# Performance work log

Hardware: AMD Instinct MI355X
Metric: run time of the kernel (lower is better)

## Reference

```python
import jax, jax.numpy as jnp
import numpy as np

PHI = 3.1415926 * 0.3   # Cosine_fMRI default phi (data_dim=-1 -> A=1)
MIN_NORM = 1e-15
PROJ_EPS = 4e-3         # float32 eps used by hyperbolic project


def _project(x, c):
    # Clip to the Poincare ball of curvature c (norm over last dim).
    norm = jnp.maximum(jnp.linalg.norm(x, axis=-1, keepdims=True), MIN_NORM)
    maxnorm = (1.0 - PROJ_EPS) / jnp.sqrt(c)
    return jnp.where(norm > maxnorm, x / norm * maxnorm, x)


def _logmap0(x, c):
    sqrt_c = jnp.sqrt(c)
    norm = jnp.maximum(jnp.linalg.norm(x, axis=-1, keepdims=True), MIN_NORM)
    arg = jnp.clip(sqrt_c * norm, -1.0 + MIN_NORM, 1.0 - MIN_NORM)
    return jnp.arctanh(arg) / (sqrt_c * norm) * x


def _fkernel(x, c):
    return _logmap0(_project(x, c), c)


def _act(x, a):
    # F.relu(x) + a * cos(x + phi)  (Cosine_fMRI with A=1)
    return jax.nn.relu(x) + a * jnp.cos(x + PHI)


def _corr_abs(data):
    # data: [B, T, N]; per-sample |corrcoef| between ROIs -> [B, N, N]
    xm = data - jnp.mean(data, axis=1, keepdims=True)
    cov = jnp.einsum('btn,btm->bnm', xm, xm)
    d = jnp.sqrt(jnp.diagonal(cov, axis1=-2, axis2=-1))  # [B, N]
    corr = cov / (d[:, :, None] * d[:, None, :])
    return jnp.abs(jnp.nan_to_num(corr))


def _normalize_adj(adj):
    # D^-1/2 (A+I) D^-1/2 per block (block-diag structure -> batched dense)
    B, N, _ = adj.shape
    A = adj + jnp.eye(N, dtype=adj.dtype)
    dinv = jnp.power(jnp.sum(A, axis=-1), -0.5)  # [B, N]
    return dinv[:, :, None] * A * dinv[:, None, :]


def setup_inputs() -> dict:
    key = jax.random.key(0)
    ks = jax.random.split(key, 3)
    B, T, N, H = 256, 240, 264, 256
    data = jax.random.normal(ks[0], (B, T, N), dtype=jnp.float32)
    # kaiming_uniform-style init for GCN weights
    b1w = np.sqrt(6.0 / N)
    b2w = np.sqrt(6.0 / H)
    W1 = jax.random.uniform(ks[1], (N, H), jnp.float32, -b1w, b1w)
    W2 = jax.random.uniform(ks[2], (H, H), jnp.float32, -b2w, b2w)
    b1 = jnp.zeros((H,), jnp.float32)
    b2 = jnp.zeros((H,), jnp.float32)
    return {"data": data, "W1": W1, "b1": b1, "W2": W2, "b2": b2}


def reference(data, W1, b1, W2, b2):
    c = jnp.float32(1.0)
    a = jnp.float32(0.5)  # a_fMRI
    adj = _corr_abs(data)          # [B, N, N]; also the input features
    L = _normalize_adj(adj)        # [B, N, N]
    # GCN layer 1: L @ (fea @ W1) + b1  (batched == block-diag sparse.mm)
    x1 = jnp.einsum('bij,bjh->bih', L, adj @ W1) + b1
    g1 = _act(_fkernel(x1, c), a)
    x2 = jnp.einsum('bij,bjh->bih', L, g1 @ W2) + b2
    g2 = _act(_fkernel(x2, c), a)  # [B, N, H]
    return g2, adj
```

## Files before the change

### kernel.cpp

```cpp
#include <hip/hip_runtime.h>
#include <hip/hip_bf16.h>
#include <math.h>

#define B_ 256
#define T_ 240
#define N_ 264
#define H_ 256
#define BN_ (B_ * N_)
#define PHI_ 0.94247778f
#define MAXNORM_ 0.996f

typedef short short8 __attribute__((ext_vector_type(8)));
typedef float f32x4 __attribute__((ext_vector_type(4)));
typedef unsigned short ushort4v __attribute__((ext_vector_type(4)));

__device__ inline unsigned short f2bf(float f) {
  __hip_bfloat16 h = __float2bfloat16(f);
  return *reinterpret_cast<unsigned short*>(&h);
}
__device__ inline float bf2f(unsigned short u) {
  unsigned int x = ((unsigned int)u) << 16;
  return __uint_as_float(x);
}

__global__ __launch_bounds__(256) void stats_kernel(
    const float* __restrict__ data, float* __restrict__ mean, float* __restrict__ rd) {
  int b = blockIdx.x;
  const float* db = data + (size_t)b * T_ * N_;
  for (int n = threadIdx.x; n < N_; n += blockDim.x) {
    float s = 0.f, ss = 0.f;
    for (int t = 0; t < T_; ++t) {
      float v = db[(size_t)t * N_ + n];
      s += v; ss += v * v;
    }
    float m = s / (float)T_;
    float var = ss - s * m;
    float d = sqrtf(fmaxf(var, 0.f));
    mean[b * N_ + n] = m;
    rd[b * N_ + n] = (d > 0.f) ? (1.f / d) : 0.f;
  }
}

__global__ __launch_bounds__(256) void zT_kernel(
    const float* __restrict__ data, const float* __restrict__ mean,
    const float* __restrict__ rd, unsigned short* __restrict__ z) {
  int b = blockIdx.y;
  int n0 = blockIdx.x * 64;
  __shared__ unsigned short zl[64][242];
  int lane = threadIdx.x & 63, wv = threadIdx.x >> 6;
  int n = n0 + lane;
  float m = 0.f, r = 0.f;
  if (n < N_) { m = mean[b * N_ + n]; r = rd[b * N_ + n]; }
  for (int t = wv; t < T_; t += 4) {
    float v = (n < N_) ? data[((size_t)b * T_ + t) * N_ + n] : 0.f;
    zl[lane][t] = f2bf((v - m) * r);
  }
  __syncthreads();
  int tid = threadIdx.x;
  for (int rr = 0; rr < 64; ++rr) {
    int nn = n0 + rr;
    if (nn >= N_) break;
    unsigned short val = (tid < T_) ? zl[rr][tid] : (unsigned short)0;
    z[((size_t)b * N_ + nn) * 256 + tid] = val;
  }
}

__global__ __launch_bounds__(256) void wtrans_kernel(
    const float* __restrict__ W, unsigned short* __restrict__ WT,
    int Jv, int Jpad) {
  int jt = blockIdx.x * 64, ht = blockIdx.y * 64;
  __shared__ float tile[64][65];
  int tid = threadIdx.x;
  for (int idx = tid; idx < 4096; idx += 256) {
    int jr = idx >> 6, hr = idx & 63;
    int j = jt + jr;
    tile[jr][hr] = (j < Jv) ? W[(size_t)j * H_ + ht + hr] : 0.f;
  }
  __syncthreads();
  for (int idx = tid; idx < 4096; idx += 256) {
    int hr = idx >> 6, jr = idx & 63;
    int j = jt + jr;
    if (j < Jpad) WT[(size_t)(ht + hr) * Jpad + j] = f2bf(tile[jr][hr]);
  }
}

__global__ __launch_bounds__(256) void dinv_kernel(
    const float* __restrict__ adj, float* __restrict__ dinv) {
  int row  = blockIdx.x * 4 + (threadIdx.x >> 6);
  int lane = threadIdx.x & 63;
  const float* r = adj + (size_t)row * N_;
  float s = 0.f;
  for (int j = lane; j < N_; j += 64) s += r[j];
#pragma unroll
  for (int off = 32; off; off >>= 1) s += __shfl_down(s, off);
  if (lane == 0) dinv[row] = 1.f / sqrtf(s + 1.f);
}

template<int EPI>
__global__ __launch_bounds__(256) void mfma_gemm_kernel(
    const unsigned short* __restrict__ A, int lda, long sA,
    const unsigned short* __restrict__ Bm, int ldb, long sB,
    int ksteps,
    float* __restrict__ outF, unsigned short* __restrict__ outB,
    const float* __restrict__ dinv, const float* __restrict__ bias) {
  int b = blockIdx.z;
  int i0 = blockIdx.y * 64;
  int n0 = blockIdx.x * 256;
  int tid = threadIdx.x;
  int w = tid >> 6, lane = tid & 63, g = lane >> 4, l4 = lane & 15;

  __shared__ short8 AsV[4 * 64];
  __shared__ short8 BsV[4 * 256];

  const unsigned short* Ab = A + (size_t)b * sA;
  const unsigned short* Bb = Bm + (size_t)b * sB;

  f32x4 acc[4][4];
#pragma unroll
  for (int x = 0; x < 4; ++x)
#pragma unroll
    for (int y = 0; y < 4; ++y) acc[x][y] = (f32x4){0.f, 0.f, 0.f, 0.f};

  int arow = tid >> 2, akg = tid & 3;
  for (int ks = 0; ks < ksteps; ++ks) {
    int k0 = ks * 32;
    short8 av = *(const short8*)(Ab + (size_t)(i0 + arow) * lda + k0 + akg * 8);
    short8 bv[4];
#pragma unroll
    for (int it = 0; it < 4; ++it) {
      int nn = n0 + arow + it * 64;
      bv[it] = *(const short8*)(Bb + (size_t)nn * ldb + k0 + akg * 8);
    }
    __syncthreads();
    AsV[akg * 64 + arow] = av;
#pragma unroll
    for (int it = 0; it < 4; ++it) BsV[akg * 256 + arow + it * 64] = bv[it];
    __syncthreads();
    short8 af[4], bfr[4];
#pragma unroll
    for (int fr = 0; fr < 4; ++fr) af[fr] = AsV[g * 64 + fr * 16 + l4];
#pragma unroll
    for (int fc = 0; fc < 4; ++fc) bfr[fc] = BsV[g * 256 + w * 64 + fc * 16 + l4];
#pragma unroll
    for (int fr = 0; fr < 4; ++fr)
#pragma unroll
      for (int fc = 0; fc < 4; ++fc)
        acc[fr][fc] = __builtin_amdgcn_mfma_f32_16x16x32_bf16(af[fr], bfr[fc], acc[fr][fc], 0, 0, 0);
  }

  if constexpr (EPI == 0) {
#pragma unroll
    for (int fr = 0; fr < 4; ++fr) {
      int rb = i0 + fr * 16 + g * 4;
#pragma unroll
      for (int fc = 0; fc < 4; ++fc) {
        int j = n0 + w * 64 + fc * 16 + l4;
#pragma unroll
        for (int reg = 0; reg < 4; ++reg) {
          int i = rb + reg;
          float v = fabsf(acc[fr][fc][reg]);
          if (i < N_ && j < N_) outF[((size_t)b * N_ + i) * N_ + j] = v;
          if (i < N_ && j < 288) outB[((size_t)b * N_ + i) * 288 + j] = f2bf(j < N_ ? v : 0.f);
        }
      }
    }
  }

  if constexpr (EPI == 1) {
#pragma unroll
    for (int fr = 0; fr < 4; ++fr) {
      int rb = i0 + fr * 16 + g * 4;
      if (rb < 288) {
        float dv[4];
#pragma unroll
        for (int reg = 0; reg < 4; ++reg) {
          int j = rb + reg;
          dv[reg] = (j < N_) ? dinv[b * N_ + j] : 0.f;
        }
#pragma unroll
        for (int fc = 0; fc < 4; ++fc) {
          int col = w * 64 + fc * 16 + l4;
          ushort4v pk;
#pragma unroll
          for (int reg = 0; reg < 4; ++reg)
            pk[reg] = f2bf(dv[reg] * acc[fr][fc][reg]);
          *(ushort4v*)(outB + ((size_t)b * H_ + col) * 288 + rb) = pk;
        }
      }
    }
  }

  if constexpr (EPI >= 2) {
    __shared__ float rs[64][4];
    float ratio[4][4];
#pragma unroll
    for (int fr = 0; fr < 4; ++fr) {
      int rb = i0 + fr * 16 + g * 4;
      float din[4];
#pragma unroll
      for (int reg = 0; reg < 4; ++reg) din[reg] = dinv[b * N_ + rb + reg];
#pragma unroll
      for (int fc = 0; fc < 4; ++fc) {
        int col = w * 64 + fc * 16 + l4;
        ushort4v dy = *(const ushort4v*)(Bb + (size_t)col * ldb + rb);
        float bias_v = bias[col];
#pragma unroll
        for (int reg = 0; reg < 4; ++reg) {
          float x = din[reg] * (acc[fr][fc][reg] + bf2f(dy[reg])) + bias_v;
          acc[fr][fc][reg] = x;
        }
      }
    }
#pragma unroll
    for (int fr = 0; fr < 4; ++fr) {
#pragma unroll
      for (int reg = 0; reg < 4; ++reg) {
        float s = 0.f;
#pragma unroll
        for (int fc = 0; fc < 4; ++fc) { float x = acc[fr][fc][reg]; s += x * x; }
        s += __shfl_xor(s, 1); s += __shfl_xor(s, 2);
        s += __shfl_xor(s, 4); s += __shfl_xor(s, 8);
        if (l4 == 0) rs[fr * 16 + g * 4 + reg][w] = s;
      }
    }
    __syncthreads();
#pragma unroll
    for (int fr = 0; fr < 4; ++fr)
#pragma unroll
      for (int reg = 0; reg < 4; ++reg) {
        int r = fr * 16 + g * 4 + reg;
        float tot = rs[r][0] + rs[r][1] + rs[r][2] + rs[r][3];
        float norm = fmaxf(sqrtf(tot), 1e-15f);
        float scale = (norm > MAXNORM_) ? (MAXNORM_ / norm) : 1.0f;
        float pn = fmaxf(fminf(norm, MAXNORM_), 1e-15f);
        ratio[fr][reg] = atanhf(pn) / pn * scale;
      }
#pragma unroll
    for (int fr = 0; fr < 4; ++fr) {
      int rb = i0 + fr * 16 + g * 4;
#pragma unroll
      for (int fc = 0; fc < 4; ++fc) {
        int col = w * 64 + fc * 16 + l4;
#pragma unroll
        for (int reg = 0; reg < 4; ++reg) {
          int row = rb + reg;
          if (row < N_) {
            float y = ratio[fr][reg] * acc[fr][fc][reg];
            float o = fmaxf(y, 0.f) + 0.5f * __cosf(y + PHI_);
            if constexpr (EPI == 2) outB[((size_t)b * N_ + row) * H_ + col] = f2bf(o);
            else                    outF[((size_t)b * N_ + row) * H_ + col] = o;
          }
        }
      }
    }
  }
}

extern "C" void kernel_launch(void* const* d_in, const int* in_sizes, int n_in,
                              void* d_out, int out_size, void* d_ws, size_t ws_size,
                              hipStream_t stream) {
  const float* data = (const float*)d_in[0];
  const float* W1   = (const float*)d_in[1];
  const float* b1   = (const float*)d_in[2];
  const float* W2   = (const float*)d_in[3];
  const float* b2   = (const float*)d_in[4];

  float* g2   = (float*)d_out;
  float* adjF = g2 + (size_t)B_ * N_ * H_;

  float* ws_f = (float*)d_ws;
  float* mean = ws_f;
  float* rd   = ws_f + BN_;
  float* dinv = ws_f + 2 * BN_;
  unsigned short* region1 = (unsigned short*)(ws_f + 3 * BN_);
  unsigned short* z    = region1;
  unsigned short* YT   = region1;
  unsigned short* W1T  = region1 + (size_t)B_ * H_ * 288;
  unsigned short* W2T  = W1T + (size_t)H_ * 288;
  unsigned short* adjB = W2T + (size_t)H_ * H_;
  unsigned short* g1bf = (unsigned short*)d_out;

  stats_kernel<<<B_, 256, 0, stream>>>(data, mean, rd);
  zT_kernel<<<dim3(5, B_), 256, 0, stream>>>(data, mean, rd, z);
  wtrans_kernel<<<dim3(5, 4), 256, 0, stream>>>(W1, W1T, N_, 288);
  wtrans_kernel<<<dim3(4, 4), 256, 0, stream>>>(W2, W2T, H_, 256);
  mfma_gemm_kernel<0><<<dim3(2, 5, B_), 256, 0, stream>>>(
      z, 256, (long)N_ * 256, z, 256, (long)N_ * 256, 8, adjF, adjB, nullptr, nullptr);
  dinv_kernel<<<BN_ / 4, 256, 0, stream>>>(adjF, dinv);
  mfma_gemm_kernel<1><<<dim3(1, 5, B_), 256, 0, stream>>>(
      adjB, 288, (long)N_ * 288, W1T, 288, 0L, 9, nullptr, YT, dinv, nullptr);
  mfma_gemm_kernel<2><<<dim3(1, 5, B_), 256, 0, stream>>>(
      adjB, 288, (long)N_ * 288, YT, 288, (long)H_ * 288, 9, nullptr, g1bf, dinv, b1);
  mfma_gemm_kernel<1><<<dim3(1, 5, B_), 256, 0, stream>>>(
      g1bf, 256, (long)N_ * 256, W2T, 256, 0L, 8, nullptr, YT, dinv, nullptr);
  mfma_gemm_kernel<3><<<dim3(1, 5, B_), 256, 0, stream>>>(
      adjB, 288, (long)N_ * 288, YT, 288, (long)H_ * 288, 9, g2, nullptr, dinv, b2);
}
```

Measured before the change: 551.1 us.

## Fuse stats into transpose, fold degree sums into corr GEMM, swizzle LDS

Merges the per-ROI mean/std computation into the z-transpose kernel via an LDS-staged tile. It also removes the separate dinv pass by atomically accumulating row sums of |corr| in the first GEMM epilogue, and computes 1/sqrt(1+sum) on the fly in later epilogues. The GEMM gains an XOR-swizzled LDS layout to cut bank conflicts, an XCD-aware workgroup remapping, clamped out-of-range A rows, and skipping of MFMA work for waves whose B columns are fully out of range. This adds a memset and float atomics (nondeterministic summation order), and re-evaluates sqrt per epilogue.

```diff
diff --git a/kernel.cpp b/kernel.cpp
--- a/kernel.cpp
+++ b/kernel.cpp
@@ -23,45 +23,45 @@
   return __uint_as_float(x);
 }
 
-__global__ __launch_bounds__(256) void stats_kernel(
-    const float* __restrict__ data, float* __restrict__ mean, float* __restrict__ rd) {
-  int b = blockIdx.x;
-  const float* db = data + (size_t)b * T_ * N_;
-  for (int n = threadIdx.x; n < N_; n += blockDim.x) {
+__device__ inline int swz16(int row, int kg) {
+  return row * 4 + ((kg ^ (row >> 1)) & 3);
+}
+
+__global__ __launch_bounds__(256) void zTs_kernel(
+    const float* __restrict__ data, unsigned short* __restrict__ z) {
+  int b = blockIdx.y;
+  int n0 = blockIdx.x * 64;
+  __shared__ float ld[240 * 65];
+  __shared__ float ps[4][64], pq[4][64];
+  __shared__ float mS[64], rS[64];
+  int tid = threadIdx.x, lane = tid & 63, wv = tid >> 6;
+  int n = n0 + lane;
+  bool nv = n < N_;
+  for (int t = wv; t < T_; t += 4)
+    ld[t * 65 + lane] = nv ? data[((size_t)b * T_ + t) * N_ + n] : 0.f;
+  __syncthreads();
+  {
+    int col = tid & 63, q = tid >> 6;
     float s = 0.f, ss = 0.f;
-    for (int t = 0; t < T_; ++t) {
-      float v = db[(size_t)t * N_ + n];
-      s += v; ss += v * v;
-    }
+    for (int t = q * 60; t < q * 60 + 60; ++t) { float v = ld[t * 65 + col]; s += v; ss += v * v; }
+    ps[q][col] = s; pq[q][col] = ss;
+  }
+  __syncthreads();
+  if (tid < 64) {
+    float s  = ps[0][tid] + ps[1][tid] + ps[2][tid] + ps[3][tid];
+    float ss = pq[0][tid] + pq[1][tid] + pq[2][tid] + pq[3][tid];
     float m = s / (float)T_;
     float var = ss - s * m;
     float d = sqrtf(fmaxf(var, 0.f));
-    mean[b * N_ + n] = m;
-    rd[b * N_ + n] = (d > 0.f) ? (1.f / d) : 0.f;
-  }
-}
-
-__global__ __launch_bounds__(256) void zT_kernel(
-    const float* __restrict__ data, const float* __restrict__ mean,
-    const float* __restrict__ rd, unsigned short* __restrict__ z) {
-  int b = blockIdx.y;
-  int n0 = blockIdx.x * 64;
-  __shared__ unsigned short zl[64][242];
-  int lane = threadIdx.x & 63, wv = threadIdx.x >> 6;
-  int n = n0 + lane;
-  float m = 0.f, r = 0.f;
-  if (n < N_) { m = mean[b * N_ + n]; r = rd[b * N_ + n]; }
-  for (int t = wv; t < T_; t += 4) {
-    float v = (n < N_) ? data[((size_t)b * T_ + t) * N_ + n] : 0.f;
-    zl[lane][t] = f2bf((v - m) * r);
+    mS[tid] = m;
+    rS[tid] = (d > 0.f) ? (1.f / d) : 0.f;
   }
   __syncthreads();
-  int tid = threadIdx.x;
-  for (int rr = 0; rr < 64; ++rr) {
-    int nn = n0 + rr;
-    if (nn >= N_) break;
-    unsigned short val = (tid < T_) ? zl[rr][tid] : (unsigned short)0;
-    z[((size_t)b * N_ + nn) * 256 + tid] = val;
+  int nrows = min(64, N_ - n0);
+  for (int rr = 0; rr < nrows; ++rr) {
+    float m = mS[rr], r = rS[rr];
+    unsigned short val = (tid < T_) ? f2bf((ld[tid * 65 + rr] - m) * r) : (unsigned short)0;
+    z[((size_t)(b * N_ + n0 + rr)) * 256 + tid] = val;
   }
 }
 
@@ -84,33 +84,28 @@
   }
 }
 
-__global__ __launch_bounds__(256) void dinv_kernel(
-    const float* __restrict__ adj, float* __restrict__ dinv) {
-  int row  = blockIdx.x * 4 + (threadIdx.x >> 6);
-  int lane = threadIdx.x & 63;
-  const float* r = adj + (size_t)row * N_;
-  float s = 0.f;
-  for (int j = lane; j < N_; j += 64) s += r[j];
-#pragma unroll
-  for (int off = 32; off; off >>= 1) s += __shfl_down(s, off);
-  if (lane == 0) dinv[row] = 1.f / sqrtf(s + 1.f);
-}
-
 template<int EPI>
 __global__ __launch_bounds__(256) void mfma_gemm_kernel(
-    const unsigned short* __restrict__ A, int lda, long sA,
-    const unsigned short* __restrict__ Bm, int ldb, long sB,
+    const unsigned short* __restrict__ A, int lda, long sA, int rowsA,
+    const unsigned short* __restrict__ Bm, int ldb, long sB, int validB,
     int ksteps,
     float* __restrict__ outF, unsigned short* __restrict__ outB,
-    const float* __restrict__ dinv, const float* __restrict__ bias) {
-  int b = blockIdx.z;
-  int i0 = blockIdx.y * 64;
-  int n0 = blockIdx.x * 256;
+    float* __restrict__ dsum, const float* __restrict__ bias) {
+  int gx = gridDim.x, gy = gridDim.y;
+  int flat = (blockIdx.z * gy + blockIdx.y) * gx + blockIdx.x;
+  int nwg = gx * gy * gridDim.z;
+  int q8 = nwg >> 3;
+  int id = (flat & 7) * q8 + (flat >> 3);
+  int bx = id % gx; int tq = id / gx;
+  int b = tq / gy;
+  int i0 = (tq % gy) * 64;
+  int n0 = bx * 256;
+
   int tid = threadIdx.x;
   int w = tid >> 6, lane = tid & 63, g = lane >> 4, l4 = lane & 15;
 
-  __shared__ short8 AsV[4 * 64];
-  __shared__ short8 BsV[4 * 256];
+  __shared__ short8 AsV[256];
+  __shared__ short8 BsV[1024];
 
   const unsigned short* Ab = A + (size_t)b * sA;
   const unsigned short* Bb = Bm + (size_t)b * sB;
@@ -122,36 +117,45 @@
     for (int y = 0; y < 4; ++y) acc[x][y] = (f32x4){0.f, 0.f, 0.f, 0.f};
 
   int arow = tid >> 2, akg = tid & 3;
+  int rA = min(i0 + arow, rowsA - 1);
+  const unsigned short* Aptr = Ab + (size_t)rA * lda + akg * 8;
+  bool wactive = (n0 + w * 64) < validB;
+  const short8 zero8 = {};
+
   for (int ks = 0; ks < ksteps; ++ks) {
     int k0 = ks * 32;
-    short8 av = *(const short8*)(Ab + (size_t)(i0 + arow) * lda + k0 + akg * 8);
+    short8 av = *(const short8*)(Aptr + k0);
     short8 bv[4];
 #pragma unroll
     for (int it = 0; it < 4; ++it) {
       int nn = n0 + arow + it * 64;
-      bv[it] = *(const short8*)(Bb + (size_t)nn * ldb + k0 + akg * 8);
+      bv[it] = (nn < validB) ? *(const short8*)(Bb + (size_t)nn * ldb + k0 + akg * 8) : zero8;
     }
     __syncthreads();
-    AsV[akg * 64 + arow] = av;
-#pragma unroll
-    for (int it = 0; it < 4; ++it) BsV[akg * 256 + arow + it * 64] = bv[it];
+    AsV[swz16(arow, akg)] = av;
+#pragma unroll
+    for (int it = 0; it < 4; ++it) BsV[swz16(arow + it * 64, akg)] = bv[it];
     __syncthreads();
-    short8 af[4], bfr[4];
-#pragma unroll
-    for (int fr = 0; fr < 4; ++fr) af[fr] = AsV[g * 64 + fr * 16 + l4];
-#pragma unroll
-    for (int fc = 0; fc < 4; ++fc) bfr[fc] = BsV[g * 256 + w * 64 + fc * 16 + l4];
-#pragma unroll
-    for (int fr = 0; fr < 4; ++fr)
-#pragma unroll
-      for (int fc = 0; fc < 4; ++fc)
-        acc[fr][fc] = __builtin_amdgcn_mfma_f32_16x16x32_bf16(af[fr], bfr[fc], acc[fr][fc], 0, 0, 0);
+    if (wactive) {
+      short8 af[4], bfr[4];
+#pragma unroll
+      for (int fr = 0; fr < 4; ++fr) af[fr] = AsV[swz16(fr * 16 + l4, g)];
+#pragma unroll
+      for (int fc = 0; fc < 4; ++fc) bfr[fc] = BsV[swz16(w * 64 + fc * 16 + l4, g)];
+#pragma unroll
+      for (int fr = 0; fr < 4; ++fr)
+#pragma unroll
+        for (int fc = 0; fc < 4; ++fc)
+          acc[fr][fc] = __builtin_amdgcn_mfma_f32_16x16x32_bf16(af[fr], bfr[fc], acc[fr][fc], 0, 0, 0);
+    }
   }
 
   if constexpr (EPI == 0) {
+    __shared__ float rsum[64][4];
 #pragma unroll
     for (int fr = 0; fr < 4; ++fr) {
       int rb = i0 + fr * 16 + g * 4;
+      float sr[4] = {0.f, 0.f, 0.f, 0.f};
 #pragma unroll
       for (int fc = 0; fc < 4; ++fc) {
         int j = n0 + w * 64 + fc * 16 + l4;
@@ -161,8 +165,23 @@
           float v = fabsf(acc[fr][fc][reg]);
           if (i < N_ && j < N_) outF[((size_t)b * N_ + i) * N_ + j] = v;
           if (i < N_ && j < 288) outB[((size_t)b * N_ + i) * 288 + j] = f2bf(j < N_ ? v : 0.f);
-        }
-      }
+          if (j < N_) sr[reg] += v;
+        }
+      }
+#pragma unroll
+      for (int reg = 0; reg < 4; ++reg) {
+        float s = sr[reg];
+        s += __shfl_xor(s, 1); s += __shfl_xor(s, 2);
+        s += __shfl_xor(s, 4); s += __shfl_xor(s, 8);
+        if (l4 == 0) rsum[fr * 16 + g * 4 + reg][w] = s;
+      }
+    }
+    __syncthreads();
+    if (tid < 64) {
+      int i = i0 + tid;
+      if (i < N_)
+        atomicAdd(&dsum[(size_t)b * N_ + i],
+                  rsum[tid][0] + rsum[tid][1] + rsum[tid][2] + rsum[tid][3]);
     }
   }
 
@@ -175,7 +194,7 @@
 #pragma unroll
         for (int reg = 0; reg < 4; ++reg) {
           int j = rb + reg;
-          dv[reg] = (j < N_) ? dinv[b * N_ + j] : 0.f;
+          dv[reg] = (j < N_) ? (1.f / sqrtf(1.f + dsum[(size_t)b * N_ + j])) : 0.f;
         }
 #pragma unroll
         for (int fc = 0; fc < 4; ++fc) {
@@ -196,13 +215,17 @@
 #pragma unroll
     for (int fr = 0; fr < 4; ++fr) {
       int rb = i0 + fr * 16 + g * 4;
+      int rbc = min(rb, 284);
       float din[4];
 #pragma unroll
-      for (int reg = 0; reg < 4; ++reg) din[reg] = dinv[b * N_ + rb + reg];
+      for (int reg = 0; reg < 4; ++reg) {
+        int ic = min(rb + reg, N_ - 1);
+        din[reg] = 1.f / sqrtf(1.f + dsum[(size_t)b * N_ + ic]);
+      }
 #pragma unroll
       for (int fc = 0; fc < 4; ++fc) {
         int col = w * 64 + fc * 16 + l4;
-        ushort4v dy = *(const ushort4v*)(Bb + (size_t)col * ldb + rb);
+        ushort4v dy = *(const ushort4v*)(Bb + (size_t)col * ldb + rbc);
         float bias_v = bias[col];
 #pragma unroll
         for (int reg = 0; reg < 4; ++reg) {
@@ -269,10 +292,8 @@
   float* adjF = g2 + (size_t)B_ * N_ * H_;
 
   float* ws_f = (float*)d_ws;
-  float* mean = ws_f;
-  float* rd   = ws_f + BN_;
-  float* dinv = ws_f + 2 * BN_;
-  unsigned short* region1 = (unsigned short*)(ws_f + 3 * BN_);
+  float* dsum = ws_f;
+  unsigned short* region1 = (unsigned short*)(ws_f + BN_);
   unsigned short* z    = region1;
   unsigned short* YT   = region1;
   unsigned short* W1T  = region1 + (size_t)B_ * H_ * 288;
@@ -280,19 +301,23 @@
   unsigned short* adjB = W2T + (size_t)H_ * H_;
   unsigned short* g1bf = (unsigned short*)d_out;
 
-  stats_kernel<<<B_, 256, 0, stream>>>(data, mean, rd);
-  zT_kernel<<<dim3(5, B_), 256, 0, stream>>>(data, mean, rd, z);
+  hipMemsetAsync(dsum, 0, BN_ * sizeof(float), stream);
+  zTs_kernel<<<dim3(5, B_), 256, 0, stream>>>(data, z);
   wtrans_kernel<<<dim3(5, 4), 256, 0, stream>>>(W1, W1T, N_, 288);
   wtrans_kernel<<<dim3(4, 4), 256, 0, stream>>>(W2, W2T, H_, 256);
   mfma_gemm_kernel<0><<<dim3(2, 5, B_), 256, 0, stream>>>(
-      z, 256, (long)N_ * 256, z, 256, (long)N_ * 256, 8, adjF, adjB, nullptr, nullptr);
-  dinv_kernel<<<BN_ / 4, 256, 0, stream>>>(adjF, dinv);
+      z, 256, (long)N_ * 256, N_, z, 256, (long)N_ * 256, N_, 8,
+      adjF, adjB, dsum, nullptr);
   mfma_gemm_kernel<1><<<dim3(1, 5, B_), 256, 0, stream>>>(
-      adjB, 288, (long)N_ * 288, W1T, 288, 0L, 9, nullptr, YT, dinv, nullptr);
+      adjB, 288, (long)N_ * 288, N_, W1T, 288, 0L, 256, 9,
+      nullptr, YT, dsum, nullptr);
   mfma_gemm_kernel<2><<<dim3(1, 5, B_), 256, 0, stream>>>(
-      adjB, 288, (long)N_ * 288, YT, 288, (long)H_ * 288, 9, nullptr, g1bf, dinv, b1);
+      adjB, 288, (long)N_ * 288, N_, YT, 288, (long)H_ * 288, 256, 9,
+      nullptr, g1bf, dsum, b1);
   mfma_gemm_kernel<1><<<dim3(1, 5, B_), 256, 0, stream>>>(
-      g1bf, 256, (long)N_ * 256, W2T, 256, 0L, 8, nullptr, YT, dinv, nullptr);
+      g1bf, 256, (long)N_ * 256, N_, W2T, 256, 0L, 256, 8,
+      nullptr, YT, dsum, nullptr);
   mfma_gemm_kernel<3><<<dim3(1, 5, B_), 256, 0, stream>>>(
-      adjB, 288, (long)N_ * 288, YT, 288, (long)H_ * 288, 9, g2, nullptr, dinv, b2);
-}
+      adjB, 288, (long)N_ * 288, N_, YT, 288, (long)H_ * 288, 256, 9,
+      g2, nullptr, dsum, b2);
+}
```

Result: slower. 730.6 us (+32.6%).
